# Optimization experiments

Measured on AMD Instinct MI355X. Metric: run time of the kernel, lower is better.

Reference implementation:

```python
import jax, jax.numpy as jnp
import numpy as np

B, T, D, H = 2, 4096, 768, 12
DK = D // H

def setup_inputs() -> dict:
    key = jax.random.key(0)
    ks = jax.random.split(key, 5)
    scale = 1.0 / np.sqrt(D)
    x = jax.random.normal(ks[0], (B, T, D), dtype=jnp.float32)
    WQ = jax.random.normal(ks[1], (D, D), dtype=jnp.float32) * scale
    WK = jax.random.normal(ks[2], (D, D), dtype=jnp.float32) * scale
    WV = jax.random.normal(ks[3], (D, D), dtype=jnp.float32) * scale
    Wproj = jax.random.normal(ks[4], (D, D), dtype=jnp.float32) * scale
    return {"x": x, "WQ": WQ, "WK": WK, "WV": WV, "Wproj": Wproj}

def reference(x, WQ, WK, WV, Wproj):
    # Weights stored as [in, out] (torch Linear weight transposed): y = x @ W
    def split_heads(y):
        return y.reshape(B, T, H, DK).transpose(0, 2, 1, 3)  # [B,H,T,DK]
    Q = split_heads(x @ WQ)
    K = split_heads(x @ WK)
    V = split_heads(x @ WV)
    score = jnp.einsum('bhqd,bhkd->bhqk', Q, K) * (DK ** -0.5)  # [B,H,T,T]
    attn = jax.nn.softmax(score, axis=-1)
    out = jnp.einsum('bhqk,bhkd->bhqd', attn, V)  # [B,H,T,DK]
    out = out.transpose(0, 2, 1, 3).reshape(B, T, D)
    return out @ Wproj
```

## Files before the change

### kernel.cpp

```cpp
#include <hip/hip_runtime.h>
#include <stdint.h>

#define B_ 2
#define T_ 4096
#define D_ 768
#define H_ 12
#define DK_ 64
#define BH_ 24

typedef unsigned short u16;
typedef unsigned int u32;
typedef __bf16 bf16x8 __attribute__((ext_vector_type(8)));
typedef float f32x4 __attribute__((ext_vector_type(4)));
typedef short s16x8 __attribute__((ext_vector_type(8)));

__device__ __forceinline__ float exp2_raw(float x) {
#if __has_builtin(__builtin_amdgcn_exp2f)
    return __builtin_amdgcn_exp2f(x);
#else
    float y; asm("v_exp_f32 %0, %1" : "=v"(y) : "v"(x)); return y;
#endif
}

__device__ __forceinline__ f32x4 mfma16(bf16x8 a, bf16x8 b, f32x4 c) {
    return __builtin_amdgcn_mfma_f32_16x16x32_bf16(a, b, c, 0, 0, 0);
}

__device__ __forceinline__ u16 f2bf(float f) {
    union { float f; u32 u; } v; v.f = f;
    u32 r = v.u + 0x7FFFu + ((v.u >> 16) & 1u);
    return (u16)(r >> 16);
}

__device__ __forceinline__ u32 pack2bf(float lo, float hi) {
    union { float f; u32 u; } a, b; a.f = lo; b.f = hi;
    return __builtin_amdgcn_perm(b.u + 0x8000u, a.u + 0x8000u, 0x07060302u);
}

__device__ __forceinline__ void gll16(const u16* g, u16* l) {
    __builtin_amdgcn_global_load_lds(
        (const __attribute__((address_space(1))) u32*)g,
        (__attribute__((address_space(3))) u32*)l, 16, 0, 0);
}

__global__ __launch_bounds__(256) void convert_x_kernel(
    const float* __restrict__ x, u16* __restrict__ xb)
{
    int i = (blockIdx.x * 256 + threadIdx.x) * 8;
    float4 a = *(const float4*)&x[i];
    float4 b = *(const float4*)&x[i + 4];
    uint4 dd;
    dd.x = pack2bf(a.x, a.y); dd.y = pack2bf(a.z, a.w);
    dd.z = pack2bf(b.x, b.y); dd.w = pack2bf(b.z, b.w);
    *(uint4*)&xb[i] = dd;
}

__global__ __launch_bounds__(256) void wtrans_kernel(
    const float* __restrict__ w0, const float* __restrict__ w1,
    const float* __restrict__ w2, const float* __restrict__ w3,
    u16* __restrict__ out)
{
    __shared__ u16 tile[32][33];
    const float* src = (blockIdx.z == 0) ? w0 : (blockIdx.z == 1) ? w1 : (blockIdx.z == 2) ? w2 : w3;
    u16* dst = out + (size_t)blockIdx.z * D_ * D_;
    int tx = threadIdx.x, ty = threadIdx.y;
    int x0 = blockIdx.x * 32, y0 = blockIdx.y * 32;
    for (int i = ty; i < 32; i += 8) tile[i][tx] = f2bf(src[(size_t)(y0 + i) * D_ + x0 + tx]);
    __syncthreads();
    for (int i = ty; i < 32; i += 8) dst[(size_t)(x0 + i) * D_ + y0 + tx] = tile[tx][i];
}

template<int MODE>
__global__ __launch_bounds__(256) void gemm_bt(
    const u16* __restrict__ A, const u16* __restrict__ Bt, void* __restrict__ outv)
{
    __shared__ u16 As[128 * 64];
    __shared__ u16 Bs[128 * 64];
    const int K = 768;
    int tid = threadIdx.x;
    int lane = tid & 63, wave = tid >> 6;
    int r = lane & 15, quad = lane >> 4;
    int rx = r & 7;
    int m0 = blockIdx.y * 128, n0 = blockIdx.x * 128;
    int wrow = (wave >> 1) * 64, wcol = (wave & 1) * 64;

    int srow = wave * 32 + (lane >> 3);
    int scol = ((lane & 7) ^ (lane >> 3)) * 8;
    const u16* Ag = A + (size_t)(m0 + srow) * K + scol;
    const u16* Bg = Bt + (size_t)(n0 + srow) * K + scol;

    f32x4 acc[4][4];
    #pragma unroll
    for (int i = 0; i < 4; i++)
        #pragma unroll
        for (int j = 0; j < 4; j++)
            #pragma unroll
            for (int e = 0; e < 4; e++) acc[i][j][e] = 0.f;

    for (int k0 = 0; k0 < K; k0 += 64) {
        __syncthreads();
        #pragma unroll
        for (int j = 0; j < 4; j++) {
            gll16(Ag + (size_t)j * 8 * K + k0, As + (wave * 32 + j * 8) * 64);
            gll16(Bg + (size_t)j * 8 * K + k0, Bs + (wave * 32 + j * 8) * 64);
        }
        __syncthreads();
        #pragma unroll
        for (int ks = 0; ks < 2; ks++) {
            int swz = ((ks * 4 + quad) ^ rx) * 8;
            bf16x8 af[4], bfr[4];
            #pragma unroll
            for (int mi = 0; mi < 4; mi++)
                af[mi] = *(const bf16x8*)&As[(wrow + mi * 16 + r) * 64 + swz];
            #pragma unroll
            for (int ni = 0; ni < 4; ni++)
                bfr[ni] = *(const bf16x8*)&Bs[(wcol + ni * 16 + r) * 64 + swz];
            #pragma unroll
            for (int mi = 0; mi < 4; mi++)
                #pragma unroll
                for (int ni = 0; ni < 4; ni++)
                    acc[mi][ni] = mfma16(af[mi], bfr[ni], acc[mi][ni]);
        }
    }

    if (MODE == 0) {
        u16* out = (u16*)outv;
        int which = n0 / D_;
        int nb = n0 % D_;
        const size_t HS = (size_t)B_ * H_ * T_ * DK_;
        if (which == 2) {
            u16* vt = out + 2 * HS;
            #pragma unroll
            for (int mi = 0; mi < 4; mi++) {
                int mg = m0 + wrow + mi * 16 + quad * 4;
                int b = mg >> 12, t = mg & 4095;
                #pragma unroll
                for (int ni = 0; ni < 4; ni++) {
                    int ng = nb + wcol + ni * 16 + r;
                    int h = ng >> 6, dk = ng & 63;
                    uint2 d;
                    d.x = pack2bf(acc[mi][ni][0], acc[mi][ni][1]);
                    d.y = pack2bf(acc[mi][ni][2], acc[mi][ni][3]);
                    *(uint2*)&vt[(((size_t)(b * H_ + h)) * DK_ + dk) * T_ + t] = d;
                }
            }
        } else {
            const float cf = (which == 0) ? 0.18033688011112042f : 1.0f;
            size_t wbase = (size_t)which * HS;
            #pragma unroll
            for (int mi = 0; mi < 4; mi++) {
                #pragma unroll
                for (int ni = 0; ni < 4; ni++) {
                    int ng = nb + wcol + ni * 16 + r;
                    int h = ng >> 6, dk = ng & 63;
                    #pragma unroll
                    for (int e = 0; e < 4; e++) {
                        int mg = m0 + wrow + mi * 16 + quad * 4 + e;
                        int b = mg >> 12, t = mg & 4095;
                        out[wbase + (((size_t)(b * H_ + h)) * T_ + t) * DK_ + dk]
                            = f2bf(acc[mi][ni][e] * cf);
                    }
                }
            }
        }
    } else {
        float* out = (float*)outv;
        #pragma unroll
        for (int mi = 0; mi < 4; mi++)
            #pragma unroll
            for (int ni = 0; ni < 4; ni++)
                #pragma unroll
                for (int e = 0; e < 4; e++)
                    out[(size_t)(m0 + wrow + mi * 16 + quad * 4 + e) * D_ + n0 + wcol + ni * 16 + r]
                        = acc[mi][ni][e];
    }
}

__global__ __launch_bounds__(256, 3) void attn_kernel(
    const u16* __restrict__ Q, const u16* __restrict__ K,
    const u16* __restrict__ VT, float* __restrict__ pO, float* __restrict__ pL)
{
    __shared__ u16 Ks[64 * 64];
    __shared__ u16 Vs[64 * 64];
    __shared__ u16 Pt[256 * 64];

    int tid = threadIdx.x;
    int lane = tid & 63, w = tid >> 6;
    int r = lane & 15, quad = lane >> 4;
    int rx = r & 7;
    int bh = blockIdx.y;
    int q0 = blockIdx.x * 256;
    int z = blockIdx.z;

    bf16x8 qf[4][2];
    #pragma unroll
    for (int qi = 0; qi < 4; qi++) {
        const u16* Qb = Q + ((size_t)bh * T_ + q0 + w * 64 + qi * 16 + r) * DK_;
        qf[qi][0] = *(const bf16x8*)(Qb + quad * 8);
        qf[qi][1] = *(const bf16x8*)(Qb + 32 + quad * 8);
    }

    bf16x8 ones;
    #pragma unroll
    for (int j = 0; j < 8; j++) ones[j] = (__bf16)1.0f;

    f32x4 o[4][4];
    f32x4 lacc[4];
    #pragma unroll
    for (int qi = 0; qi < 4; qi++) {
        #pragma unroll
        for (int e = 0; e < 4; e++) lacc[qi][e] = 0.f;
        #pragma unroll
        for (int n = 0; n < 4; n++)
            #pragma unroll
            for (int e = 0; e < 4; e++) o[qi][n][e] = 0.f;
    }

    u16* Pw = &Pt[w * 64 * 64];
    int kb0 = z * (T_ / 2), kb1 = kb0 + T_ / 2;

    for (int kb = kb0; kb < kb1; kb += 64) {
        __syncthreads();
        #pragma unroll
        for (int i = 0; i < 2; i++) {
            int c = tid + i * 256;
            int row = c >> 3, gc = c & 7;
            int lc = gc ^ (row & 7);
            *(bf16x8*)&Ks[row * 64 + lc * 8] =
                *(const bf16x8*)&K[((size_t)bh * T_ + kb + row) * DK_ + gc * 8];
            *(bf16x8*)&Vs[row * 64 + lc * 8] =
                *(const bf16x8*)&VT[((size_t)bh * DK_ + row) * T_ + kb + gc * 8];
        }
        __syncthreads();

        #pragma unroll
        for (int n = 0; n < 4; n++) {
            int krow = n * 16 + r;
            bf16x8 kf0 = *(const bf16x8*)&Ks[krow * 64 + ((quad ^ rx)) * 8];
            bf16x8 kf1 = *(const bf16x8*)&Ks[krow * 64 + (((4 + quad) ^ rx)) * 8];
            int c8 = 2 * n + (quad >> 1);
            #pragma unroll
            for (int qi = 0; qi < 4; qi++) {
                f32x4 zz;
                #pragma unroll
                for (int e = 0; e < 4; e++) zz[e] = 0.f;
                zz = mfma16(kf0, qf[qi][0], zz);
                zz = mfma16(kf1, qf[qi][1], zz);
                float p0 = exp2_raw(zz[0]), p1 = exp2_raw(zz[1]);
                float p2 = exp2_raw(zz[2]), p3 = exp2_raw(zz[3]);
                uint2 d;
                d.x = pack2bf(p0, p1);
                d.y = pack2bf(p2, p3);
                *(uint2*)&Pw[(qi * 16 + r) * 64 + (c8 ^ rx) * 8 + (quad & 1) * 4] = d;
            }
        }

        #pragma unroll
        for (int ks2 = 0; ks2 < 2; ks2++) {
            int swz = ((ks2 * 4 + quad) ^ rx) * 8;
            bf16x8 vf[4];
            #pragma unroll
            for (int ndk = 0; ndk < 4; ndk++)
                vf[ndk] = *(const bf16x8*)&Vs[(ndk * 16 + r) * 64 + swz];
            #pragma unroll
            for (int qi = 0; qi < 4; qi++) {
                bf16x8 pf = *(const bf16x8*)&Pw[(qi * 16 + r) * 64 + swz];
                lacc[qi] = mfma16(ones, pf, lacc[qi]);
                #pragma unroll
                for (int ndk = 0; ndk < 4; ndk++)
                    o[qi][ndk] = mfma16(vf[ndk], pf, o[qi][ndk]);
            }
        }
    }

    const size_t SP = (size_t)BH_ * T_ * DK_;
    #pragma unroll
    for (int qi = 0; qi < 4; qi++) {
        int q = q0 + w * 64 + qi * 16 + r;
        float* base = pO + (size_t)z * SP + ((size_t)bh * T_ + q) * DK_;
        #pragma unroll
        for (int ndk = 0; ndk < 4; ndk++)
            *(f32x4*)&base[ndk * 16 + quad * 4] = o[qi][ndk];
    }
    if (quad == 0) {
        #pragma unroll
        for (int qi = 0; qi < 4; qi++)
            pL[(size_t)z * BH_ * T_ + (size_t)bh * T_ + q0 + w * 64 + qi * 16 + r]
                = lacc[qi][0];
    }
}

__global__ __launch_bounds__(256) void combine_kernel(
    const float* __restrict__ pO, const float* __restrict__ pL, u16* __restrict__ AO)
{
    const size_t SP = (size_t)BH_ * T_ * DK_;
    int bh = blockIdx.y;
    int b = bh / H_, h = bh % H_;
    int q = blockIdx.x * 64 + (threadIdx.x >> 2);
    int dk0 = (threadIdx.x & 3) * 16;
    size_t idx = ((size_t)bh * T_ + q) * DK_ + dk0;
    float l0 = pL[(size_t)bh * T_ + q];
    float l1 = pL[(size_t)BH_ * T_ + (size_t)bh * T_ + q];
    float inv = 1.0f / (l0 + l1);
    u16* dst = AO + ((size_t)b * T_ + q) * D_ + h * DK_ + dk0;
    #pragma unroll
    for (int i = 0; i < 2; i++) {
        float4 a0 = *(const float4*)&pO[idx + i * 8];
        float4 a1 = *(const float4*)&pO[idx + i * 8 + 4];
        float4 b0 = *(const float4*)&pO[SP + idx + i * 8];
        float4 b1 = *(const float4*)&pO[SP + idx + i * 8 + 4];
        uint4 dd;
        dd.x = pack2bf((a0.x + b0.x) * inv, (a0.y + b0.y) * inv);
        dd.y = pack2bf((a0.z + b0.z) * inv, (a0.w + b0.w) * inv);
        dd.z = pack2bf((a1.x + b1.x) * inv, (a1.y + b1.y) * inv);
        dd.w = pack2bf((a1.z + b1.z) * inv, (a1.w + b1.w) * inv);
        *(uint4*)&dst[i * 8] = dd;
    }
}

extern "C" void kernel_launch(void* const* d_in, const int* in_sizes, int n_in,
                              void* d_out, int out_size, void* d_ws, size_t ws_size,
                              hipStream_t stream)
{
    const float* x  = (const float*)d_in[0];
    const float* wq = (const float*)d_in[1];
    const float* wk = (const float*)d_in[2];
    const float* wv = (const float*)d_in[3];
    const float* wp = (const float*)d_in[4];

    u16* ws = (u16*)d_ws;
    const size_t XS = (size_t)B_ * T_ * D_;
    const size_t WT = (size_t)D_ * D_;
    const size_t HS = (size_t)B_ * H_ * T_ * DK_;
    u16* xb = ws;
    u16* wt = xb + XS;
    u16* q  = wt + 4 * WT;
    u16* k  = q + HS;
    u16* vt = k + HS;
    u16* ao = vt + HS;
    float* pL = (float*)(ao + HS);
    float* pO = pL + 2 * (size_t)BH_ * T_;

    convert_x_kernel<<<dim3(3072), 256, 0, stream>>>(x, xb);
    wtrans_kernel<<<dim3(24, 24, 4), dim3(32, 8), 0, stream>>>(wq, wk, wv, wp, wt);
    gemm_bt<0><<<dim3(18, 64), 256, 0, stream>>>(xb, wt, q);
    attn_kernel<<<dim3(16, 24, 2), 256, 0, stream>>>(q, k, vt, pO, pL);
    combine_kernel<<<dim3(64, 24), 256, 0, stream>>>(pO, pL, ao);
    gemm_bt<1><<<dim3(6, 64), 256, 0, stream>>>(ao, wt + 3 * WT, d_out);
}
```

Before: 293.4 us.

## Prefetch next K/V tile into registers and raise priority around MFMA blocks

Global loads of the next K and V tile go into registers during the current iteration and are written to shared memory after the barrier, so global latency overlaps with compute. __syncthreads is replaced with explicit lgkmcnt waits plus s_barrier under sched barriers. MFMA sections are wrapped in s_setprio, and the manual bf16 packing is replaced with native __bf16 conversion. This adds register pressure, and the native conversion may round differently from the old pack routine.

```diff
diff --git a/kernel.cpp b/kernel.cpp
--- a/kernel.cpp
+++ b/kernel.cpp
@@ -11,6 +11,7 @@
 typedef unsigned short u16;
 typedef unsigned int u32;
 typedef __bf16 bf16x8 __attribute__((ext_vector_type(8)));
+typedef __bf16 bf16x4 __attribute__((ext_vector_type(4)));
 typedef float f32x4 __attribute__((ext_vector_type(4)));
 typedef short s16x8 __attribute__((ext_vector_type(8)));
 
@@ -219,19 +220,43 @@
     u16* Pw = &Pt[w * 64 * 64];
     int kb0 = z * (T_ / 2), kb1 = kb0 + T_ / 2;
 
+    int c1 = tid + 256;
+    int row0 = tid >> 3, gc0 = tid & 7;
+    int row1 = c1 >> 3,  gc1 = c1 & 7;
+    int lc0 = gc0 ^ (row0 & 7);
+    int lc1 = gc1 ^ (row1 & 7);
+    const u16* Kg0 = K + ((size_t)bh * T_ + row0) * DK_ + gc0 * 8;
+    const u16* Kg1 = K + ((size_t)bh * T_ + row1) * DK_ + gc1 * 8;
+    const u16* Vg0 = VT + ((size_t)bh * DK_ + row0) * T_ + gc0 * 8;
+    const u16* Vg1 = VT + ((size_t)bh * DK_ + row1) * T_ + gc1 * 8;
+
+    bf16x8 kr0 = *(const bf16x8*)(Kg0 + (size_t)kb0 * DK_);
+    bf16x8 kr1 = *(const bf16x8*)(Kg1 + (size_t)kb0 * DK_);
+    bf16x8 vr0 = *(const bf16x8*)(Vg0 + kb0);
+    bf16x8 vr1 = *(const bf16x8*)(Vg1 + kb0);
+
     for (int kb = kb0; kb < kb1; kb += 64) {
-        __syncthreads();
-        #pragma unroll
-        for (int i = 0; i < 2; i++) {
-            int c = tid + i * 256;
-            int row = c >> 3, gc = c & 7;
-            int lc = gc ^ (row & 7);
-            *(bf16x8*)&Ks[row * 64 + lc * 8] =
-                *(const bf16x8*)&K[((size_t)bh * T_ + kb + row) * DK_ + gc * 8];
-            *(bf16x8*)&Vs[row * 64 + lc * 8] =
-                *(const bf16x8*)&VT[((size_t)bh * DK_ + row) * T_ + kb + gc * 8];
-        }
-        __syncthreads();
+        asm volatile("s_waitcnt lgkmcnt(0)" ::: "memory");
+        __builtin_amdgcn_sched_barrier(0);
+        __builtin_amdgcn_s_barrier();
+        __builtin_amdgcn_sched_barrier(0);
+
+        *(bf16x8*)&Ks[row0 * 64 + lc0 * 8] = kr0;
+        *(bf16x8*)&Ks[row1 * 64 + lc1 * 8] = kr1;
+        *(bf16x8*)&Vs[row0 * 64 + lc0 * 8] = vr0;
+        *(bf16x8*)&Vs[row1 * 64 + lc1 * 8] = vr1;
+
+        if (kb + 64 < kb1) {
+            kr0 = *(const bf16x8*)(Kg0 + (size_t)(kb + 64) * DK_);
+            kr1 = *(const bf16x8*)(Kg1 + (size_t)(kb + 64) * DK_);
+            vr0 = *(const bf16x8*)(Vg0 + (kb + 64));
+            vr1 = *(const bf16x8*)(Vg1 + (kb + 64));
+        }
+
+        asm volatile("s_waitcnt lgkmcnt(0)" ::: "memory");
+        __builtin_amdgcn_sched_barrier(0);
+        __builtin_amdgcn_s_barrier();
+        __builtin_amdgcn_sched_barrier(0);
 
         #pragma unroll
         for (int n = 0; n < 4; n++) {
@@ -244,14 +269,14 @@
                 f32x4 zz;
                 #pragma unroll
                 for (int e = 0; e < 4; e++) zz[e] = 0.f;
+                __builtin_amdgcn_s_setprio(1);
                 zz = mfma16(kf0, qf[qi][0], zz);
                 zz = mfma16(kf1, qf[qi][1], zz);
-                float p0 = exp2_raw(zz[0]), p1 = exp2_raw(zz[1]);
-                float p2 = exp2_raw(zz[2]), p3 = exp2_raw(zz[3]);
-                uint2 d;
-                d.x = pack2bf(p0, p1);
-                d.y = pack2bf(p2, p3);
-                *(uint2*)&Pw[(qi * 16 + r) * 64 + (c8 ^ rx) * 8 + (quad & 1) * 4] = d;
+                __builtin_amdgcn_s_setprio(0);
+                bf16x4 pv;
+                #pragma unroll
+                for (int e = 0; e < 4; e++) pv[e] = (__bf16)exp2_raw(zz[e]);
+                *(bf16x4*)&Pw[(qi * 16 + r) * 64 + (c8 ^ rx) * 8 + (quad & 1) * 4] = pv;
             }
         }
 
@@ -265,10 +290,12 @@
             #pragma unroll
             for (int qi = 0; qi < 4; qi++) {
                 bf16x8 pf = *(const bf16x8*)&Pw[(qi * 16 + r) * 64 + swz];
+                __builtin_amdgcn_s_setprio(1);
                 lacc[qi] = mfma16(ones, pf, lacc[qi]);
                 #pragma unroll
                 for (int ndk = 0; ndk < 4; ndk++)
                     o[qi][ndk] = mfma16(vf[ndk], pf, o[qi][ndk]);
+                __builtin_amdgcn_s_setprio(0);
             }
         }
     }
```

After: 326.1 us. 11.1% more time.

## Keep attention probabilities in registers by permuting K rows to match MFMA layout

Applied to the files above, without the earlier changes.

Removes the shared-memory staging buffer for the softmax probability tile. K rows are chosen so that each lane's QK^T MFMA outputs, once packed into bf16x8, line up with the B-operand layout the PV MFMA expects, and the LDS swizzle is changed to match. This drops the P store and reload and 32 KB of LDS per block, which may allow higher occupancy. In exchange the K-load index math and swizzle are more complex, and correctness depends on the row permutation being applied consistently to K and V.

```diff
diff --git a/kernel.cpp b/kernel.cpp
--- a/kernel.cpp
+++ b/kernel.cpp
@@ -182,12 +182,10 @@
 {
     __shared__ u16 Ks[64 * 64];
     __shared__ u16 Vs[64 * 64];
-    __shared__ u16 Pt[256 * 64];
 
     int tid = threadIdx.x;
     int lane = tid & 63, w = tid >> 6;
     int r = lane & 15, quad = lane >> 4;
-    int rx = r & 7;
     int bh = blockIdx.y;
     int q0 = blockIdx.x * 256;
     int z = blockIdx.z;
@@ -216,8 +214,8 @@
             for (int e = 0; e < 4; e++) o[qi][n][e] = 0.f;
     }
 
-    u16* Pw = &Pt[w * 64 * 64];
     int kb0 = z * (T_ / 2), kb1 = kb0 + T_ / 2;
+    int rb = ((r >> 2) * 8) + (r & 3);
 
     for (int kb = kb0; kb < kb1; kb += 64) {
         __syncthreads();
@@ -225,7 +223,8 @@
         for (int i = 0; i < 2; i++) {
             int c = tid + i * 256;
             int row = c >> 3, gc = c & 7;
-            int lc = gc ^ (row & 7);
+            int fr = ((row >> 3) & 1) * 4 + (row & 3);
+            int lc = gc ^ fr;
             *(bf16x8*)&Ks[row * 64 + lc * 8] =
                 *(const bf16x8*)&K[((size_t)bh * T_ + kb + row) * DK_ + gc * 8];
             *(bf16x8*)&Vs[row * 64 + lc * 8] =
@@ -234,37 +233,37 @@
         __syncthreads();
 
         #pragma unroll
-        for (int n = 0; n < 4; n++) {
-            int krow = n * 16 + r;
-            bf16x8 kf0 = *(const bf16x8*)&Ks[krow * 64 + ((quad ^ rx)) * 8];
-            bf16x8 kf1 = *(const bf16x8*)&Ks[krow * 64 + (((4 + quad) ^ rx)) * 8];
-            int c8 = 2 * n + (quad >> 1);
+        for (int s = 0; s < 2; s++) {
+            int rowA = s * 32 + rb;
+            int rowB = rowA + 4;
+            int fA = ((rowA >> 3) & 1) * 4 + (rowA & 3);
+            int fB = ((rowB >> 3) & 1) * 4 + (rowB & 3);
+            bf16x8 kA0 = *(const bf16x8*)&Ks[rowA * 64 + (quad ^ fA) * 8];
+            bf16x8 kA1 = *(const bf16x8*)&Ks[rowA * 64 + (((4 + quad) ^ fA)) * 8];
+            bf16x8 kB0 = *(const bf16x8*)&Ks[rowB * 64 + (quad ^ fB) * 8];
+            bf16x8 kB1 = *(const bf16x8*)&Ks[rowB * 64 + (((4 + quad) ^ fB)) * 8];
+            bf16x8 vf[4];
+            #pragma unroll
+            for (int ndk = 0; ndk < 4; ndk++) {
+                int row = ndk * 16 + r;
+                int fv = ((row >> 3) & 1) * 4 + (row & 3);
+                vf[ndk] = *(const bf16x8*)&Vs[row * 64 + (((s * 4 + quad) ^ fv)) * 8];
+            }
             #pragma unroll
             for (int qi = 0; qi < 4; qi++) {
-                f32x4 zz;
-                #pragma unroll
-                for (int e = 0; e < 4; e++) zz[e] = 0.f;
-                zz = mfma16(kf0, qf[qi][0], zz);
-                zz = mfma16(kf1, qf[qi][1], zz);
-                float p0 = exp2_raw(zz[0]), p1 = exp2_raw(zz[1]);
-                float p2 = exp2_raw(zz[2]), p3 = exp2_raw(zz[3]);
-                uint2 d;
-                d.x = pack2bf(p0, p1);
-                d.y = pack2bf(p2, p3);
-                *(uint2*)&Pw[(qi * 16 + r) * 64 + (c8 ^ rx) * 8 + (quad & 1) * 4] = d;
-            }
-        }
-
-        #pragma unroll
-        for (int ks2 = 0; ks2 < 2; ks2++) {
-            int swz = ((ks2 * 4 + quad) ^ rx) * 8;
-            bf16x8 vf[4];
-            #pragma unroll
-            for (int ndk = 0; ndk < 4; ndk++)
-                vf[ndk] = *(const bf16x8*)&Vs[(ndk * 16 + r) * 64 + swz];
-            #pragma unroll
-            for (int qi = 0; qi < 4; qi++) {
-                bf16x8 pf = *(const bf16x8*)&Pw[(qi * 16 + r) * 64 + swz];
+                f32x4 zA, zB;
+                #pragma unroll
+                for (int e = 0; e < 4; e++) { zA[e] = 0.f; zB[e] = 0.f; }
+                zA = mfma16(kA0, qf[qi][0], zA);
+                zA = mfma16(kA1, qf[qi][1], zA);
+                zB = mfma16(kB0, qf[qi][0], zB);
+                zB = mfma16(kB1, qf[qi][1], zB);
+                union { uint4 u; bf16x8 v; } pu;
+                pu.u.x = pack2bf(exp2_raw(zA[0]), exp2_raw(zA[1]));
+                pu.u.y = pack2bf(exp2_raw(zA[2]), exp2_raw(zA[3]));
+                pu.u.z = pack2bf(exp2_raw(zB[0]), exp2_raw(zB[1]));
+                pu.u.w = pack2bf(exp2_raw(zB[2]), exp2_raw(zB[3]));
+                bf16x8 pf = pu.v;
                 lacc[qi] = mfma16(ones, pf, lacc[qi]);
                 #pragma unroll
                 for (int ndk = 0; ndk < 4; ndk++)
```

After: 281.6 us. -4.0%, faster.
